# Kernel optimization log

Measured on AMD Instinct MI355X. Metric: run time of the kernel, lower is better.

Reference implementation:

```python
import jax, jax.numpy as jnp
import numpy as np
from jax import lax

DN = ('NHWC', 'HWIO', 'NHWC')


def conv_same(x, w):
    return lax.conv_general_dilated(x, w, window_strides=(1, 1), padding='SAME',
                                    dimension_numbers=DN)


def dwconv(x, w):
    # w: (kh, kw, F, 1) TF depthwise layout -> HWIO (kh, kw, 1, F), groups=F
    F = w.shape[2]
    return lax.conv_general_dilated(x, jnp.transpose(w, (0, 1, 3, 2)),
                                    window_strides=(1, 1), padding='SAME',
                                    dimension_numbers=DN, feature_group_count=F)


def hard_sigmoid(x):
    return jnp.clip(0.2 * x + 0.5, 0.0, 1.0)


def setup_inputs() -> dict:
    key = jax.random.key(0)
    ks = jax.random.split(key, 10)
    B, H, W, Cin, F = 16, 128, 128, 64, 64
    s = 0.05
    return {
        'inputs': jax.random.normal(ks[0], (B, H, W, Cin), jnp.float32),
        'h0': jax.random.normal(ks[1], (B, H, W, F), jnp.float32),
        'c0': jax.random.normal(ks[2], (B, H, W, F), jnp.float32),
        'm0': jax.random.normal(ks[3], (B, H, W, F), jnp.float32),
        'kernel': jax.random.normal(ks[4], (3, 3, Cin, 4 * F), jnp.float32) * s,
        'recurrent_kernel': jax.random.normal(ks[5], (3, 3, F, 4 * F), jnp.float32) * s,
        'bias': jnp.concatenate([jnp.zeros((F,), jnp.float32),
                                 jnp.ones((F,), jnp.float32),
                                 jnp.zeros((2 * F,), jnp.float32)]),
        'sa_kernel': jax.random.normal(ks[6], (1, 1, F, 5), jnp.float32) * s,
        'kernel_z': jax.random.normal(ks[7], (3, 3, 2, F), jnp.float32) * s,
        'depth_wise_kernel': jax.random.normal(ks[8], (3, 3, F, 6), jnp.float32) * s,
        'sa_bias': jnp.zeros((3 * F,), jnp.float32),
    }


def reference(inputs, h0, c0, m0, kernel, recurrent_kernel, bias, sa_kernel,
              kernel_z, depth_wise_kernel, sa_bias):
    F = h0.shape[-1]
    # --- ConvLSTM gates (no dropout: all four gates share the same input, so
    # a single fused conv over the 4F-channel kernel is the same math) ---
    xz = conv_same(inputs, kernel) + bias  # [B,H,W,4F]
    hz = conv_same(h0, recurrent_kernel)   # [B,H,W,4F]
    z = xz + hz
    zi_, zf_, zc_, zo_ = jnp.split(z, 4, axis=-1)
    i = hard_sigmoid(zi_)
    f = hard_sigmoid(zf_)
    c = f * c0 + i * jnp.tanh(zc_)
    o = hard_sigmoid(zo_)
    h = o * jnp.tanh(c)  # [B,H,W,F]

    # --- Self-attention memory (SAM) module; 1x1 convs -> channel contractions ---
    w = sa_kernel[0, 0]  # [F,5]
    v_h = jnp.einsum('bhwc,c->bhw', h, w[:, 0])
    k_h = jnp.einsum('bhwc,c->bhw', h, w[:, 1])
    q_h = jnp.einsum('bhwc,c->bhw', h, w[:, 2])
    k_m = jnp.einsum('bhwc,c->bhw', m0, w[:, 3])
    v_m = jnp.einsum('bhwc,c->bhw', m0, w[:, 4])

    alpha_m = jax.nn.softmax(jnp.matmul(q_h, k_m), axis=-1)  # [B,H,H] (H==W)
    alpha_h = jax.nn.softmax(jnp.matmul(q_h, k_h), axis=-1)
    z_m = jnp.matmul(alpha_m, v_m)  # [B,H,W]
    z_h = jnp.matmul(alpha_h, v_h)

    zi = conv_same(jnp.stack([z_h, z_m], axis=-1), kernel_z)  # [B,H,W,F]

    dw = depth_wise_kernel  # [3,3,F,6]
    b_i, b_g, b_o = jnp.split(sa_bias, 3)
    i2 = jax.nn.sigmoid(dwconv(zi, dw[..., 0:1]) + dwconv(h, dw[..., 1:2]) + b_i)
    g = jnp.tanh(dwconv(zi, dw[..., 2:3]) + dwconv(h, dw[..., 3:4]) + b_g)
    o2 = jax.nn.sigmoid(dwconv(zi, dw[..., 4:5]) + dwconv(h, dw[..., 5:6]) + b_o)

    m_t = (1.0 - i2) * m0 + i2 * g
    h_hat = m_t * o2
    return h_hat, c, m_t
```

## Files before the change

### kernel.cpp

```cpp
#include <hip/hip_runtime.h>

#define BB 16
#define HH 128
#define WW 128
#define FF 64
#define NPIX (BB*HH*WW)

typedef short bf16x8 __attribute__((ext_vector_type(8)));
typedef float f32x4 __attribute__((ext_vector_type(4)));

__device__ __forceinline__ float bf2f(unsigned int u){ return __uint_as_float(u<<16); }
__device__ __forceinline__ unsigned short f2bf(float f){
  unsigned u = __float_as_uint(f);
  u += 0x7fffu + ((u>>16)&1u);
  return (unsigned short)(u>>16);
}
__device__ __forceinline__ float hsig(float x){ return fminf(fmaxf(fmaf(0.2f,x,0.5f),0.f),1.f); }
__device__ __forceinline__ float tanh_fast(float x){
  float e = __expf(2.f*x);
  return 1.f - 2.f/(e + 1.f);
}
__device__ __forceinline__ void gload_lds16(const void* g, void* l){
  __builtin_amdgcn_global_load_lds(
      (const __attribute__((address_space(1))) unsigned int*)g,
      (__attribute__((address_space(3))) unsigned int*)l, 16, 0, 0);
}

__global__ __launch_bounds__(256) void zero_pads(unsigned short* __restrict__ Xp){
  int i = blockIdx.x*256 + threadIdx.x;
  if (i >= 16*516) return;
  int b = i / 516, r = i % 516;
  int y, x;
  if (r < 130){ y = 0; x = r; }
  else if (r < 260){ y = 129; x = r-130; }
  else if (r < 388){ y = r-260+1; x = 0; }
  else { y = r-388+1; x = 129; }
  unsigned short* p = Xp + (((size_t)(b*130 + y)*130) + x)*128;
  uint4 z = {0u,0u,0u,0u};
  #pragma unroll
  for (int c=0;c<16;++c) ((uint4*)p)[c] = z;
}

__global__ __launch_bounds__(256) void prep_x(const float* __restrict__ in,
                                              const float* __restrict__ h0,
                                              unsigned short* __restrict__ Xp){
  int gi = blockIdx.x*256 + threadIdx.x;
  int pix = gi >> 4;
  int ch8 = (gi & 15) * 8;
  const float* src = (ch8 < 64) ? (in + (size_t)pix*64 + ch8)
                                : (h0 + (size_t)pix*64 + (ch8-64));
  float4 v0 = *(const float4*)src;
  float4 v1 = *(const float4*)(src+4);
  uint4 o;
  o.x = (unsigned)f2bf(v0.x) | ((unsigned)f2bf(v0.y)<<16);
  o.y = (unsigned)f2bf(v0.z) | ((unsigned)f2bf(v0.w)<<16);
  o.z = (unsigned)f2bf(v1.x) | ((unsigned)f2bf(v1.y)<<16);
  o.w = (unsigned)f2bf(v1.z) | ((unsigned)f2bf(v1.w)<<16);
  int b = pix >> 14, y = (pix >> 7) & 127, x = pix & 127;
  *(uint4*)(Xp + (((size_t)(b*130 + y+1)*130) + (x+1))*128 + ch8) = o;
}

__global__ __launch_bounds__(256) void prep_w(const float* __restrict__ kern,
                                              const float* __restrict__ rkern,
                                              unsigned short* __restrict__ Wg){
  int k = blockIdx.x;
  int n = threadIdx.x;
  int tap = k >> 7, c = k & 127;
  float v = (c < 64) ? kern[((size_t)(tap*64 + c))*256 + n]
                     : rkern[((size_t)(tap*64 + (c-64)))*256 + n];
  Wg[(size_t)n*1152 + k] = f2bf(v);
}

__global__ __launch_bounds__(256, 2) void gates_kernel(
    const unsigned short* __restrict__ Xp,
    const unsigned short* __restrict__ Wg,
    const float* __restrict__ bias,
    const float* __restrict__ c0,
    float* __restrict__ c_out,
    unsigned short* __restrict__ h_bf){
  __shared__ unsigned short As[2][130*128];
  const int gid = blockIdx.x;
  const int swz = (gid & 7)*256 + (gid >> 3);
  const int b  = swz >> 7;
  const int y  = swz & 127;
  const int tid = threadIdx.x;
  const int l = tid & 63;
  const int wid = tid >> 6;
  const int l15 = l & 15, l4 = l >> 4;
  const int n0 = wid*16 + l15;

  const unsigned short* brow[4];
  #pragma unroll
  for (int g=0; g<4; ++g) brow[g] = Wg + (size_t)(g*64 + n0)*1152 + l4*8;

  f32x4 acc[8][4];
  #pragma unroll
  for (int mf=0;mf<8;++mf)
    #pragma unroll
    for (int g=0;g<4;++g) acc[mf][g] = (f32x4){0.f,0.f,0.f,0.f};

  auto stage = [&](int buf, int dyi){
    const unsigned short* gbase = Xp + ((size_t)((b*130 + y + dyi)*130))*128;
    unsigned short* lbase = &As[buf][0];
    #pragma unroll
    for (int it=0; it<8; ++it){
      int q = it*256 + tid;
      int px = q >> 4, c = q & 15;
      int cs = c ^ (px & 7);
      gload_lds16(gbase + (size_t)px*128 + cs*8, lbase + (size_t)q*8);
    }
    if (l < 8){
      int q = 2048 + wid*8 + l;
      int px = q >> 4, c = q & 15;
      int cs = c ^ (px & 7);
      gload_lds16(gbase + (size_t)px*128 + cs*8, lbase + (size_t)q*8);
    }
  };

  stage(0, 0);
  for (int dyi = 0; dyi < 3; ++dyi){
    if (dyi < 2){
      stage((dyi+1)&1, dyi+1);
      asm volatile("s_waitcnt vmcnt(9)" ::: "memory");
    } else {
      asm volatile("s_waitcnt vmcnt(0)" ::: "memory");
    }
    __builtin_amdgcn_sched_barrier(0);
    __builtin_amdgcn_s_barrier();
    __builtin_amdgcn_sched_barrier(0);
    const unsigned short* asb = &As[dyi&1][0];
    #pragma unroll
    for (int dxi = 0; dxi < 3; ++dxi){
      const int tap = dyi*3 + dxi;
      #pragma unroll
      for (int ksc = 0; ksc < 2; ++ksc){
        bf16x8 bfr[4][2];
        #pragma unroll
        for (int g=0; g<4; ++g)
          #pragma unroll
          for (int k2=0; k2<2; ++k2)
            bfr[g][k2] = *(const bf16x8*)(brow[g] + tap*128 + (ksc*2+k2)*32);
        #pragma unroll
        for (int k2=0; k2<2; ++k2){
          const int cd = (ksc*2+k2)*4 + l4;
          #pragma unroll
          for (int mf=0; mf<8; ++mf){
            const int px = mf*16 + l15 + dxi;
            bf16x8 a = *(const bf16x8*)(asb + (size_t)px*128 + ((cd ^ (px & 7))*8));
            #pragma unroll
            for (int g=0;g<4;++g)
              acc[mf][g] = __builtin_amdgcn_mfma_f32_16x16x32_bf16(a, bfr[g][k2], acc[mf][g], 0,0,0);
          }
        }
      }
    }
    __builtin_amdgcn_sched_barrier(0);
    __builtin_amdgcn_s_barrier();
    __builtin_amdgcn_sched_barrier(0);
  }
  const float b0 = bias[n0], b1 = bias[64+n0], b2 = bias[128+n0], b3 = bias[192+n0];
  const size_t prow = (size_t)(b*128 + y)*128;
  #pragma unroll
  for (int mf=0;mf<8;++mf){
    #pragma unroll
    for (int r=0;r<4;++r){
      const int x = mf*16 + l4*4 + r;
      const size_t p = prow + x;
      const float zi_ = acc[mf][0][r] + b0;
      const float zf_ = acc[mf][1][r] + b1;
      const float zc_ = acc[mf][2][r] + b2;
      const float zo_ = acc[mf][3][r] + b3;
      const float iv = hsig(zi_), fv = hsig(zf_), ov = hsig(zo_);
      const float cv = fv*c0[p*64 + n0] + iv*tanh_fast(zc_);
      const float hv = ov*tanh_fast(cv);
      c_out[p*64 + n0] = cv;
      h_bf[p*64 + n0] = f2bf(hv);
    }
  }
}

__global__ __launch_bounds__(256) void qkv_kernel(
    const unsigned short* __restrict__ h_bf, const float* __restrict__ m0,
    const float* __restrict__ sak,
    float* __restrict__ q_h, float* __restrict__ k_h, float* __restrict__ v_h,
    float* __restrict__ k_m, float* __restrict__ v_m){
  __shared__ float wS[320];
  for (int i = threadIdx.x; i < 320; i += 256) wS[i] = sak[i];
  __syncthreads();
  const int p = blockIdx.x*256 + threadIdx.x;
  const unsigned short* hp = h_bf + (size_t)p*64;
  const float* mp = m0 + (size_t)p*64;
  float a0=0,a1=0,a2=0,a3=0,a4=0;
  #pragma unroll
  for (int ch = 0; ch < 64; ch += 8){
    uint4 hu = *(const uint4*)(hp + ch);
    float4 ma = *(const float4*)(mp + ch);
    float4 mb = *(const float4*)(mp + ch + 4);
    float hv[8] = { bf2f(hu.x&0xffffu), bf2f(hu.x>>16), bf2f(hu.y&0xffffu), bf2f(hu.y>>16),
                    bf2f(hu.z&0xffffu), bf2f(hu.z>>16), bf2f(hu.w&0xffffu), bf2f(hu.w>>16) };
    float mv[8] = { ma.x,ma.y,ma.z,ma.w, mb.x,mb.y,mb.z,mb.w };
    #pragma unroll
    for (int jj=0;jj<8;++jj){
      const float* w = &wS[(ch+jj)*5];
      a0 = fmaf(hv[jj], w[0], a0);
      a1 = fmaf(hv[jj], w[1], a1);
      a2 = fmaf(hv[jj], w[2], a2);
      a3 = fmaf(mv[jj], w[3], a3);
      a4 = fmaf(mv[jj], w[4], a4);
    }
  }
  v_h[p]=a0; k_h[p]=a1; q_h[p]=a2; k_m[p]=a3; v_m[p]=a4;
}

__global__ __launch_bounds__(256) void attn_kernel(
    const float* __restrict__ q_h, const float* __restrict__ k_h, const float* __restrict__ v_h,
    const float* __restrict__ k_m, const float* __restrict__ v_m,
    float* __restrict__ z_h, float* __restrict__ z_m){
  __shared__ float q2[2][128];
  __shared__ float al[2][128];
  __shared__ float redm[2][2], reds[2][2];
  const int bid = blockIdx.x;
  const int b = bid >> 5;
  const int type = (bid >> 4) & 1;
  const int rb = bid & 15;
  const float* K = (type ? k_m : k_h) + (size_t)b*16384;
  const float* V = (type ? v_m : v_h) + (size_t)b*16384;
  const float* Q = q_h + (size_t)b*16384;
  float* Z = (type ? z_m : z_h) + (size_t)b*16384;
  const int t = threadIdx.x, rg = t>>7, j = t&127, lane = t&63, hw = (t>>6)&1;
  for (int it = 0; it < 4; ++it){
    const int i = rb*8 + it*2 + rg;
    __syncthreads();
    q2[rg][j] = Q[i*128 + j];
    __syncthreads();
    float s = 0.f;
    #pragma unroll 8
    for (int w=0; w<128; ++w) s = fmaf(q2[rg][w], K[w*128 + j], s);
    float mx = s;
    #pragma unroll
    for (int o=1;o<64;o<<=1) mx = fmaxf(mx, __shfl_xor(mx, o));
    if (lane==0) redm[rg][hw] = mx;
    __syncthreads();
    mx = fmaxf(redm[rg][0], redm[rg][1]);
    float pe = __expf(s - mx);
    float sm = pe;
    #pragma unroll
    for (int o=1;o<64;o<<=1) sm += __shfl_xor(sm, o);
    if (lane==0) reds[rg][hw] = sm;
    __syncthreads();
    const float inv = 1.f/(reds[rg][0]+reds[rg][1]);
    al[rg][j] = pe*inv;
    __syncthreads();
    float z = 0.f;
    #pragma unroll 8
    for (int w=0; w<128; ++w) z = fmaf(al[rg][w], V[w*128 + j], z);
    Z[i*128 + j] = z;
  }
}

__global__ __launch_bounds__(512) void zconv_kernel(
    const float* __restrict__ z_h, const float* __restrict__ z_m,
    const float* __restrict__ kz, unsigned short* __restrict__ zi_bf){
  const int f = threadIdx.x & 63;
  const int g = threadIdx.x >> 6;
  const int row = blockIdx.x;
  const int y = row & 127;
  float w0[9], w1[9];
  #pragma unroll
  for (int tap=0; tap<9; ++tap){
    w0[tap] = kz[tap*128 + f];
    w1[tap] = kz[tap*128 + 64 + f];
  }
  const float* zhr = z_h + (size_t)row*128;
  const float* zmr = z_m + (size_t)row*128;
  const bool ym = (y > 0), yp = (y < 127);
  float az[3][3], am[3][3];
  auto ldc = [&](int x, float (&Z)[3], float (&M)[3]){
    if ((unsigned)x < 128u){
      Z[0] = ym ? zhr[x-128] : 0.f;  M[0] = ym ? zmr[x-128] : 0.f;
      Z[1] = zhr[x];                 M[1] = zmr[x];
      Z[2] = yp ? zhr[x+128] : 0.f;  M[2] = yp ? zmr[x+128] : 0.f;
    } else { Z[0]=Z[1]=Z[2]=0.f; M[0]=M[1]=M[2]=0.f; }
  };
  const int x0 = g*16;
  ldc(x0-1, az[0], am[0]);
  ldc(x0,   az[1], am[1]);
  for (int i=0; i<16; ++i){
    const int x = x0 + i;
    ldc(x+1, az[2], am[2]);
    float acc = 0.f;
    #pragma unroll
    for (int tap=0; tap<9; ++tap){
      const int dy = tap/3, dx = tap%3;
      acc = fmaf(az[dx][dy], w0[tap], acc);
      acc = fmaf(am[dx][dy], w1[tap], acc);
    }
    zi_bf[((size_t)row*128 + x)*64 + f] = f2bf(acc);
    #pragma unroll
    for (int k=0;k<3;++k){
      az[0][k]=az[1][k]; az[1][k]=az[2][k];
      am[0][k]=am[1][k]; am[1][k]=am[2][k];
    }
  }
}

__global__ __launch_bounds__(256) void final_kernel(
    const unsigned short* __restrict__ zi_bf, const unsigned short* __restrict__ h_bf,
    const float* __restrict__ m0, const float* __restrict__ dwk,
    const float* __restrict__ sab,
    float* __restrict__ hhat, float* __restrict__ m_t){
  const int f = threadIdx.x & 63;
  const int g = threadIdx.x >> 6;
  const int row = blockIdx.x;
  const int y = row & 127;
  float wv[9][6];
  #pragma unroll
  for (int tap=0;tap<9;++tap)
    #pragma unroll
    for (int jj=0;jj<6;++jj) wv[tap][jj] = dwk[(tap*64 + f)*6 + jj];
  const float bi = sab[f], bg = sab[64+f], bo = sab[128+f];
  const bool ym = (y > 0), yp = (y < 127);
  const size_t rb = (size_t)row*128;
  float vz[3][3], vh[3][3];
  auto ldc = [&](int x, float (&Z)[3], float (&H)[3]){
    if ((unsigned)x < 128u){
      const size_t base = (rb + x)*64 + f;
      Z[0] = ym ? bf2f(zi_bf[base - 8192]) : 0.f;
      H[0] = ym ? bf2f(h_bf [base - 8192]) : 0.f;
      Z[1] = bf2f(zi_bf[base]);
      H[1] = bf2f(h_bf [base]);
      Z[2] = yp ? bf2f(zi_bf[base + 8192]) : 0.f;
      H[2] = yp ? bf2f(h_bf [base + 8192]) : 0.f;
    } else { Z[0]=Z[1]=Z[2]=0.f; H[0]=H[1]=H[2]=0.f; }
  };
  const int x0 = g*32;
  ldc(x0-1, vz[0], vh[0]);
  ldc(x0,   vz[1], vh[1]);
  for (int i=0; i<32; ++i){
    const int x = x0 + i;
    ldc(x+1, vz[2], vh[2]);
    float si=0.f, sg=0.f, so=0.f;
    #pragma unroll
    for (int tap=0;tap<9;++tap){
      const int dy = tap/3, dx = tap%3;
      const float zv = vz[dx][dy], hv = vh[dx][dy];
      si = fmaf(zv, wv[tap][0], si); si = fmaf(hv, wv[tap][1], si);
      sg = fmaf(zv, wv[tap][2], sg); sg = fmaf(hv, wv[tap][3], sg);
      so = fmaf(zv, wv[tap][4], so); so = fmaf(hv, wv[tap][5], so);
    }
    const size_t p = rb + x;
    const float i2 = 1.f/(1.f+__expf(-(si+bi)));
    const float gg = tanh_fast(sg+bg);
    const float o2 = 1.f/(1.f+__expf(-(so+bo)));
    const float mv = m0[p*64+f];
    const float mt = (1.f-i2)*mv + i2*gg;
    hhat[p*64+f] = mt*o2;
    m_t[p*64+f]  = mt;
    #pragma unroll
    for (int k=0;k<3;++k){
      vz[0][k]=vz[1][k]; vz[1][k]=vz[2][k];
      vh[0][k]=vh[1][k]; vh[1][k]=vh[2][k];
    }
  }
}

extern "C" void kernel_launch(void* const* d_in, const int* in_sizes, int n_in,
                              void* d_out, int out_size, void* d_ws, size_t ws_size,
                              hipStream_t stream){
  const float* inputs = (const float*)d_in[0];
  const float* h0p    = (const float*)d_in[1];
  const float* c0p    = (const float*)d_in[2];
  const float* m0p    = (const float*)d_in[3];
  const float* kern   = (const float*)d_in[4];
  const float* rkern  = (const float*)d_in[5];
  const float* biasp  = (const float*)d_in[6];
  const float* sakp   = (const float*)d_in[7];
  const float* kzp    = (const float*)d_in[8];
  const float* dwkp   = (const float*)d_in[9];
  const float* sabp   = (const float*)d_in[10];
  float* out = (float*)d_out;
  char* ws = (char*)d_ws;

  constexpr size_t SZ_XP  = (size_t)16*130*130*128*2;
  constexpr size_t SZ_WG  = (size_t)256*1152*2;
  constexpr size_t SZ_HBF = (size_t)NPIX*64*2;
  constexpr size_t SZA    = (size_t)NPIX*4;
  constexpr size_t OFF_XP  = 0;
  constexpr size_t OFF_WG  = OFF_XP + SZ_XP;
  constexpr size_t OFF_HBF = OFF_WG + SZ_WG;
  constexpr size_t OFF_Q   = OFF_HBF + SZ_HBF;
  constexpr size_t OFF_KH  = OFF_Q  + SZA;
  constexpr size_t OFF_VH  = OFF_KH + SZA;
  constexpr size_t OFF_KM  = OFF_VH + SZA;
  constexpr size_t OFF_VM  = OFF_KM + SZA;
  constexpr size_t OFF_ZH  = OFF_VM + SZA;
  constexpr size_t OFF_ZM  = OFF_ZH + SZA;
  constexpr size_t OFF_ZI  = OFF_ZM + SZA;

  unsigned short* Xp  = (unsigned short*)(ws + OFF_XP);
  unsigned short* Wg  = (unsigned short*)(ws + OFF_WG);
  unsigned short* Hbf = (unsigned short*)(ws + OFF_HBF);
  float* Qh = (float*)(ws + OFF_Q);
  float* Kh = (float*)(ws + OFF_KH);
  float* Vh = (float*)(ws + OFF_VH);
  float* Km = (float*)(ws + OFF_KM);
  float* Vm = (float*)(ws + OFF_VM);
  float* Zh = (float*)(ws + OFF_ZH);
  float* Zm = (float*)(ws + OFF_ZM);
  unsigned short* ZIbf = (unsigned short*)(ws + OFF_ZI);

  zero_pads<<<33, 256, 0, stream>>>(Xp);
  prep_x<<<NPIX*16/256, 256, 0, stream>>>(inputs, h0p, Xp);
  prep_w<<<1152, 256, 0, stream>>>(kern, rkern, Wg);
  gates_kernel<<<2048, 256, 0, stream>>>(Xp, Wg, biasp, c0p,
                                         out + (size_t)NPIX*64, Hbf);
  qkv_kernel<<<NPIX/256, 256, 0, stream>>>(Hbf, m0p, sakp, Qh, Kh, Vh, Km, Vm);
  attn_kernel<<<512, 256, 0, stream>>>(Qh, Kh, Vh, Km, Vm, Zh, Zm);
  zconv_kernel<<<2048, 512, 0, stream>>>(Zh, Zm, kzp, ZIbf);
  final_kernel<<<2048, 256, 0, stream>>>(ZIbf, Hbf, m0p, dwkp, sabp,
                                         out, out + 2*(size_t)NPIX*64);
}
```

Before: 420.1 us.

## Fuse z-conv into final depthwise kernel via LDS halo tile; split attention accumulators

Merges the zconv and final kernels. Each block computes zi for two output rows plus a one-row halo above and below directly into shared memory, so the bf16 zi tensor no longer makes a round trip through global memory and one launch goes away. The cost is recomputing the halo rows (about 2x zconv work) and a 64KB LDS footprint per block, which lowers occupancy. The attention dot products also now use four independent accumulators to break the FMA dependency chain.

```diff
diff --git a/kernel.cpp b/kernel.cpp
--- a/kernel.cpp
+++ b/kernel.cpp
@@ -233,9 +233,15 @@
     __syncthreads();
     q2[rg][j] = Q[i*128 + j];
     __syncthreads();
-    float s = 0.f;
-    #pragma unroll 8
-    for (int w=0; w<128; ++w) s = fmaf(q2[rg][w], K[w*128 + j], s);
+    float s0=0.f, s1=0.f, s2=0.f, s3=0.f;
+    #pragma unroll
+    for (int w=0; w<128; w+=4){
+      s0 = fmaf(q2[rg][w  ], K[(w  )*128 + j], s0);
+      s1 = fmaf(q2[rg][w+1], K[(w+1)*128 + j], s1);
+      s2 = fmaf(q2[rg][w+2], K[(w+2)*128 + j], s2);
+      s3 = fmaf(q2[rg][w+3], K[(w+3)*128 + j], s3);
+    }
+    float s = (s0+s1)+(s2+s3);
     float mx = s;
     #pragma unroll
     for (int o=1;o<64;o<<=1) mx = fmaxf(mx, __shfl_xor(mx, o));
@@ -251,68 +257,84 @@
     const float inv = 1.f/(reds[rg][0]+reds[rg][1]);
     al[rg][j] = pe*inv;
     __syncthreads();
-    float z = 0.f;
-    #pragma unroll 8
-    for (int w=0; w<128; ++w) z = fmaf(al[rg][w], V[w*128 + j], z);
-    Z[i*128 + j] = z;
-  }
-}
-
-__global__ __launch_bounds__(512) void zconv_kernel(
+    float z0=0.f, z1=0.f, z2=0.f, z3=0.f;
+    #pragma unroll
+    for (int w=0; w<128; w+=4){
+      z0 = fmaf(al[rg][w  ], V[(w  )*128 + j], z0);
+      z1 = fmaf(al[rg][w+1], V[(w+1)*128 + j], z1);
+      z2 = fmaf(al[rg][w+2], V[(w+2)*128 + j], z2);
+      z3 = fmaf(al[rg][w+3], V[(w+3)*128 + j], z3);
+    }
+    Z[i*128 + j] = (z0+z1)+(z2+z3);
+  }
+}
+
+__global__ __launch_bounds__(512) void final_fused(
     const float* __restrict__ z_h, const float* __restrict__ z_m,
-    const float* __restrict__ kz, unsigned short* __restrict__ zi_bf){
-  const int f = threadIdx.x & 63;
-  const int g = threadIdx.x >> 6;
-  const int row = blockIdx.x;
-  const int y = row & 127;
-  float w0[9], w1[9];
-  #pragma unroll
-  for (int tap=0; tap<9; ++tap){
-    w0[tap] = kz[tap*128 + f];
-    w1[tap] = kz[tap*128 + 64 + f];
-  }
-  const float* zhr = z_h + (size_t)row*128;
-  const float* zmr = z_m + (size_t)row*128;
-  const bool ym = (y > 0), yp = (y < 127);
-  float az[3][3], am[3][3];
-  auto ldc = [&](int x, float (&Z)[3], float (&M)[3]){
-    if ((unsigned)x < 128u){
-      Z[0] = ym ? zhr[x-128] : 0.f;  M[0] = ym ? zmr[x-128] : 0.f;
-      Z[1] = zhr[x];                 M[1] = zmr[x];
-      Z[2] = yp ? zhr[x+128] : 0.f;  M[2] = yp ? zmr[x+128] : 0.f;
-    } else { Z[0]=Z[1]=Z[2]=0.f; M[0]=M[1]=M[2]=0.f; }
-  };
-  const int x0 = g*16;
-  ldc(x0-1, az[0], am[0]);
-  ldc(x0,   az[1], am[1]);
-  for (int i=0; i<16; ++i){
-    const int x = x0 + i;
-    ldc(x+1, az[2], am[2]);
-    float acc = 0.f;
-    #pragma unroll
-    for (int tap=0; tap<9; ++tap){
-      const int dy = tap/3, dx = tap%3;
-      acc = fmaf(az[dx][dy], w0[tap], acc);
-      acc = fmaf(am[dx][dy], w1[tap], acc);
-    }
-    zi_bf[((size_t)row*128 + x)*64 + f] = f2bf(acc);
-    #pragma unroll
-    for (int k=0;k<3;++k){
-      az[0][k]=az[1][k]; az[1][k]=az[2][k];
-      am[0][k]=am[1][k]; am[1][k]=am[2][k];
-    }
-  }
-}
-
-__global__ __launch_bounds__(256) void final_kernel(
-    const unsigned short* __restrict__ zi_bf, const unsigned short* __restrict__ h_bf,
+    const float* __restrict__ kz,
+    const unsigned short* __restrict__ h_bf,
     const float* __restrict__ m0, const float* __restrict__ dwk,
     const float* __restrict__ sab,
     float* __restrict__ hhat, float* __restrict__ m_t){
+  __shared__ unsigned short zi[4][128][64];
   const int f = threadIdx.x & 63;
   const int g = threadIdx.x >> 6;
-  const int row = blockIdx.x;
-  const int y = row & 127;
+  const int blk = blockIdx.x;
+  const int b = blk >> 6;
+  const int y0 = (blk & 63) * 2;
+
+  {
+    const int ry = g >> 1;
+    const int xh = g & 1;
+    const int yy = y0 - 1 + ry;
+    const int x0 = xh * 64;
+    if ((unsigned)yy >= 128u){
+      for (int i=0;i<64;++i) zi[ry][x0+i][f] = 0;
+    } else {
+      float w0[9], w1[9];
+      #pragma unroll
+      for (int tap=0; tap<9; ++tap){
+        w0[tap] = kz[tap*128 + f];
+        w1[tap] = kz[tap*128 + 64 + f];
+      }
+      const float* zhr = z_h + (size_t)(b*128 + yy)*128;
+      const float* zmr = z_m + (size_t)(b*128 + yy)*128;
+      const bool ym = (yy > 0), yp = (yy < 127);
+      float az[3][3], am[3][3];
+      auto ldc = [&](int x, float (&Z)[3], float (&M)[3]){
+        if ((unsigned)x < 128u){
+          Z[0] = ym ? zhr[x-128] : 0.f;  M[0] = ym ? zmr[x-128] : 0.f;
+          Z[1] = zhr[x];                 M[1] = zmr[x];
+          Z[2] = yp ? zhr[x+128] : 0.f;  M[2] = yp ? zmr[x+128] : 0.f;
+        } else { Z[0]=Z[1]=Z[2]=0.f; M[0]=M[1]=M[2]=0.f; }
+      };
+      ldc(x0-1, az[0], am[0]);
+      ldc(x0,   az[1], am[1]);
+      for (int i=0; i<64; ++i){
+        const int x = x0 + i;
+        ldc(x+1, az[2], am[2]);
+        float acc = 0.f;
+        #pragma unroll
+        for (int tap=0; tap<9; ++tap){
+          const int dy = tap/3, dx = tap%3;
+          acc = fmaf(az[dx][dy], w0[tap], acc);
+          acc = fmaf(am[dx][dy], w1[tap], acc);
+        }
+        zi[ry][x][f] = f2bf(acc);
+        #pragma unroll
+        for (int k=0;k<3;++k){
+          az[0][k]=az[1][k]; az[1][k]=az[2][k];
+          am[0][k]=am[1][k]; am[1][k]=am[2][k];
+        }
+      }
+    }
+  }
+  __syncthreads();
+
+  const int r2 = g >> 2;
+  const int xq = g & 3;
+  const int y = y0 + r2;
+  const size_t rb = (size_t)(b*128 + y)*128;
   float wv[9][6];
   #pragma unroll
   for (int tap=0;tap<9;++tap)
@@ -320,25 +342,24 @@
     for (int jj=0;jj<6;++jj) wv[tap][jj] = dwk[(tap*64 + f)*6 + jj];
   const float bi = sab[f], bg = sab[64+f], bo = sab[128+f];
   const bool ym = (y > 0), yp = (y < 127);
-  const size_t rb = (size_t)row*128;
   float vz[3][3], vh[3][3];
-  auto ldc = [&](int x, float (&Z)[3], float (&H)[3]){
+  auto ldc2 = [&](int x, float (&Z)[3], float (&H)[3]){
     if ((unsigned)x < 128u){
       const size_t base = (rb + x)*64 + f;
-      Z[0] = ym ? bf2f(zi_bf[base - 8192]) : 0.f;
-      H[0] = ym ? bf2f(h_bf [base - 8192]) : 0.f;
-      Z[1] = bf2f(zi_bf[base]);
-      H[1] = bf2f(h_bf [base]);
-      Z[2] = yp ? bf2f(zi_bf[base + 8192]) : 0.f;
-      H[2] = yp ? bf2f(h_bf [base + 8192]) : 0.f;
+      H[0] = ym ? bf2f(h_bf[base - 8192]) : 0.f;
+      H[1] = bf2f(h_bf[base]);
+      H[2] = yp ? bf2f(h_bf[base + 8192]) : 0.f;
+      Z[0] = bf2f(zi[r2  ][x][f]);
+      Z[1] = bf2f(zi[r2+1][x][f]);
+      Z[2] = bf2f(zi[r2+2][x][f]);
     } else { Z[0]=Z[1]=Z[2]=0.f; H[0]=H[1]=H[2]=0.f; }
   };
-  const int x0 = g*32;
-  ldc(x0-1, vz[0], vh[0]);
-  ldc(x0,   vz[1], vh[1]);
+  const int x0 = xq*32;
+  ldc2(x0-1, vz[0], vh[0]);
+  ldc2(x0,   vz[1], vh[1]);
   for (int i=0; i<32; ++i){
     const int x = x0 + i;
-    ldc(x+1, vz[2], vh[2]);
+    ldc2(x+1, vz[2], vh[2]);
     float si=0.f, sg=0.f, so=0.f;
     #pragma unroll
     for (int tap=0;tap<9;++tap){
@@ -395,7 +416,6 @@
   constexpr size_t OFF_VM  = OFF_KM + SZA;
   constexpr size_t OFF_ZH  = OFF_VM + SZA;
   constexpr size_t OFF_ZM  = OFF_ZH + SZA;
-  constexpr size_t OFF_ZI  = OFF_ZM + SZA;
 
   unsigned short* Xp  = (unsigned short*)(ws + OFF_XP);
   unsigned short* Wg  = (unsigned short*)(ws + OFF_WG);
@@ -407,7 +427,6 @@
   float* Vm = (float*)(ws + OFF_VM);
   float* Zh = (float*)(ws + OFF_ZH);
   float* Zm = (float*)(ws + OFF_ZM);
-  unsigned short* ZIbf = (unsigned short*)(ws + OFF_ZI);
 
   zero_pads<<<33, 256, 0, stream>>>(Xp);
   prep_x<<<NPIX*16/256, 256, 0, stream>>>(inputs, h0p, Xp);
@@ -416,7 +435,6 @@
                                          out + (size_t)NPIX*64, Hbf);
   qkv_kernel<<<NPIX/256, 256, 0, stream>>>(Hbf, m0p, sakp, Qh, Kh, Vh, Km, Vm);
   attn_kernel<<<512, 256, 0, stream>>>(Qh, Kh, Vh, Km, Vm, Zh, Zm);
-  zconv_kernel<<<2048, 512, 0, stream>>>(Zh, Zm, kzp, ZIbf);
-  final_kernel<<<2048, 256, 0, stream>>>(ZIbf, Hbf, m0p, dwkp, sabp,
-                                         out, out + 2*(size_t)NPIX*64);
-}
+  final_fused<<<1024, 512, 0, stream>>>(Zh, Zm, kzp, Hbf, m0p, dwkp, sabp,
+                                        out, out + 2*(size_t)NPIX*64);
+}
```

New measurement: 420.8 us. No clear change (+0.2%).
